# Kernel optimization log

Hardware: AMD Instinct MI355X
Metric: run time of the kernel (lower is better)

The kernel has to match this reference:

```python
import jax, jax.numpy as jnp
import numpy as np

VOCAB = 32000
HID = 1024
HEADS = 16
HEAD_DIM = HID // HEADS
LAYERS = 8
INTER = 4 * HID
ROPE_BASE = 100000.0
EPS = 1e-5


def setup_inputs() -> dict:
    key = jax.random.key(0)
    ks = jax.random.split(key, 12)
    s = 0.02
    inp = {
        'input_ids': jax.random.randint(ks[0], (2, 2048), 0, VOCAB),
        'embed_W': jax.random.normal(ks[1], (VOCAB, HID), jnp.float32) * s,
        'Wq': jax.random.normal(ks[2], (LAYERS, HID, HID), jnp.float32) * s,
        'Wk': jax.random.normal(ks[3], (LAYERS, HID, HID), jnp.float32) * s,
        'Wv': jax.random.normal(ks[4], (LAYERS, HID, HID), jnp.float32) * s,
        'Wo': jax.random.normal(ks[5], (LAYERS, HID, HID), jnp.float32) * s,
        'Wg': jax.random.normal(ks[6], (LAYERS, HID, INTER), jnp.float32) * s,
        'Wu': jax.random.normal(ks[7], (LAYERS, HID, INTER), jnp.float32) * s,
        'Wd': jax.random.normal(ks[8], (LAYERS, INTER, HID), jnp.float32) * s,
        'norm1_w': jnp.ones((LAYERS, HID), jnp.float32),
        'norm2_w': jnp.ones((LAYERS, HID), jnp.float32),
        'final_norm_w': jnp.ones((HID,), jnp.float32),
        'head_W': jax.random.normal(ks[9], (HID, VOCAB), jnp.float32) * s,
    }
    return inp


def rms_norm(x, w):
    return x * jax.lax.rsqrt(jnp.mean(x * x, axis=-1, keepdims=True) + EPS) * w


def rope_tables(seq_len):
    freq = 1.0 / (ROPE_BASE ** (jnp.arange(0, HEAD_DIM, 2, dtype=jnp.float32) / HEAD_DIM))
    ang = jnp.arange(seq_len, dtype=jnp.float32)[:, None] * freq  # [S, d/2]
    cos = jnp.concatenate([jnp.cos(ang), jnp.cos(ang)], axis=-1)  # [S, d]
    sin = jnp.concatenate([jnp.sin(ang), jnp.sin(ang)], axis=-1)
    return cos, sin


def rotate_half(x):
    h = x.shape[-1] // 2
    return jnp.concatenate([-x[..., h:], x[..., :h]], axis=-1)


def apply_rope(q, k, cos, sin):
    # q,k: [B,S,H,D]; cos,sin: [S,D] -> broadcast over heads via [:,None,:]
    c = cos[:, None, :]
    s = sin[:, None, :]
    return q * c + rotate_half(q) * s, k * c + rotate_half(k) * s


def attention(x, wq, wk, wv, wo, cos, sin, causal_mask):
    B, S, _ = x.shape
    q = (x @ wq).reshape(B, S, HEADS, HEAD_DIM)
    k = (x @ wk).reshape(B, S, HEADS, HEAD_DIM)
    v = (x @ wv).reshape(B, S, HEADS, HEAD_DIM)
    q, k = apply_rope(q, k, cos, sin)
    scores = jnp.einsum('bqhd,bkhd->bhqk', q, k) / np.sqrt(HEAD_DIM)
    scores = jnp.clip(scores, -1000.0, 1000.0)
    scores = jnp.where(causal_mask, jnp.finfo(scores.dtype).min, scores)
    w = jax.nn.softmax(scores.astype(jnp.float32), axis=-1).astype(q.dtype)
    w = jnp.clip(w, 0.0, 1.0)
    ctx = jnp.einsum('bhqk,bkhd->bqhd', w, v).reshape(B, S, HID)
    return ctx @ wo


def reference(input_ids, embed_W, Wq, Wk, Wv, Wo, Wg, Wu, Wd, norm1_w, norm2_w, final_norm_w, head_W):
    B, S = input_ids.shape
    h = embed_W[input_ids]  # [B,S,HID]
    cos, sin = rope_tables(S)
    causal_mask = jnp.triu(jnp.ones((S, S), bool), k=1)[None, None]
    for l in range(LAYERS):
        h = h + attention(rms_norm(h, norm1_w[l]), Wq[l], Wk[l], Wv[l], Wo[l], cos, sin, causal_mask)
        hn = rms_norm(h, norm2_w[l])
        h = h + (jax.nn.silu(hn @ Wg[l]) * (hn @ Wu[l])) @ Wd[l]
    h = rms_norm(h, final_norm_w)
    logits = h @ head_W
    return logits, h
```

## Files before the change

kernel.cpp:

```cpp
#include <hip/hip_runtime.h>

#define T_TOK 4096
#define SEQ   2048
#define HID   1024
#define NH    16
#define HD    64
#define INTER 4096
#define NLAYER 8
#define VOCAB 32000

typedef short short8 __attribute__((ext_vector_type(8)));
typedef float f32x4  __attribute__((ext_vector_type(4)));

__device__ __forceinline__ unsigned short f2bf(float f){
  unsigned int u = __builtin_bit_cast(unsigned int, f);
  u += 0x7fffu + ((u >> 16) & 1u);
  return (unsigned short)(u >> 16);
}
__device__ __forceinline__ float bf2f(unsigned short b){
  unsigned int u = ((unsigned int)b) << 16;
  return __builtin_bit_cast(float, u);
}

#define GLOAD_LDS16(gsrc, ldst) \
  __builtin_amdgcn_global_load_lds((const __attribute__((address_space(1))) void*)(gsrc), \
                                   (__attribute__((address_space(3))) void*)(ldst), 16, 0, 0)

__global__ __launch_bounds__(256) void embed_kernel(const int* __restrict__ ids,
                                                    const float* __restrict__ W,
                                                    float* __restrict__ h){
  int i = blockIdx.x * 256 + threadIdx.x;
  int t = i >> 8, c = i & 255;
  ((float4*)h)[i] = ((const float4*)(W + (size_t)ids[t] * HID))[c];
}

__global__ __launch_bounds__(256) void rope_tab_kernel(float* __restrict__ cosT,
                                                       float* __restrict__ sinT){
  int i = blockIdx.x * 256 + threadIdx.x;
  int s = i >> 5, f = i & 31;
  float inv = expf(-((2.0f * (float)f) / 64.0f) * logf(100000.0f));
  float ang = (float)s * inv;
  cosT[i] = cosf(ang);
  sinT[i] = sinf(ang);
}

__global__ __launch_bounds__(256) void rmsnorm_kernel(const float* __restrict__ h,
                                                      const float* __restrict__ w,
                                                      unsigned short* __restrict__ out,
                                                      float* hcopy){
  int t = blockIdx.x, tid = threadIdx.x;
  float4 v = ((const float4*)(h + (size_t)t * HID))[tid];
  float ss = v.x*v.x + v.y*v.y + v.z*v.z + v.w*v.w;
  #pragma unroll
  for (int m = 1; m < 64; m <<= 1) ss += __shfl_xor(ss, m);
  __shared__ float red[4];
  if ((tid & 63) == 0) red[tid >> 6] = ss;
  __syncthreads();
  float r = rsqrtf((red[0] + red[1] + red[2] + red[3]) * (1.0f / HID) + 1e-5f);
  float4 wv = ((const float4*)w)[tid];
  float nx = v.x * r * wv.x;
  float ny = v.y * r * wv.y;
  float nz = v.z * r * wv.z;
  float nw = v.w * r * wv.w;
  ushort4 o;
  o.x = f2bf(nx); o.y = f2bf(ny); o.z = f2bf(nz); o.w = f2bf(nw);
  ((ushort4*)(out + (size_t)t * HID))[tid] = o;
  if (hcopy){
    float4 hv; hv.x = nx; hv.y = ny; hv.z = nz; hv.w = nw;
    ((float4*)(hcopy + (size_t)t * HID))[tid] = hv;
  }
}

__global__ __launch_bounds__(256) void convert_w_qkvo(const float* __restrict__ W0,
                                                      const float* __restrict__ W1,
                                                      const float* __restrict__ W2,
                                                      const float* __restrict__ W3,
                                                      unsigned short* __restrict__ Wt){
  __shared__ unsigned short t_lds[64][72];
  const int z = blockIdx.z, sel = z >> 3, l = z & 7;
  const float* W = ((sel == 0) ? W0 : (sel == 1) ? W1 : (sel == 2) ? W2 : W3)
                 + (size_t)l * HID * HID;
  unsigned short* dst = Wt + (size_t)z * HID * HID;
  const int n0 = blockIdx.x * 64, k0 = blockIdx.y * 64;
  const int tid = threadIdx.x;
  const int tr = tid >> 4, tc = tid & 15;
  #pragma unroll
  for (int i = 0; i < 4; ++i){
    int kk = tr + i * 16;
    float4 v = *(const float4*)(W + (size_t)(k0 + kk) * HID + n0 + tc * 4);
    t_lds[tc*4+0][kk] = f2bf(v.x);
    t_lds[tc*4+1][kk] = f2bf(v.y);
    t_lds[tc*4+2][kk] = f2bf(v.z);
    t_lds[tc*4+3][kk] = f2bf(v.w);
  }
  __syncthreads();
  const int n = tid >> 2, cp = tid & 3;
  #pragma unroll
  for (int j = 0; j < 2; ++j){
    int c = cp * 2 + j;
    uint4 d = *(const uint4*)(&t_lds[n][c * 8]);
    *(uint4*)(dst + (size_t)(n0 + n) * HID + k0 + ((c ^ (n & 7)) << 3)) = d;
  }
}

__global__ __launch_bounds__(256) void convert_w_swz(const float* __restrict__ W,
                                                     unsigned short* __restrict__ Wt,
                                                     int K, int N){
  __shared__ unsigned short t_lds[64][72];
  W  += (size_t)blockIdx.z * K * N;
  Wt += (size_t)blockIdx.z * K * N;
  const int n0 = blockIdx.x * 64, k0 = blockIdx.y * 64;
  const int tid = threadIdx.x;
  const int tr = tid >> 4, tc = tid & 15;
  #pragma unroll
  for (int i = 0; i < 4; ++i){
    int kk = tr + i * 16;
    float4 v = *(const float4*)(W + (size_t)(k0 + kk) * N + n0 + tc * 4);
    t_lds[tc*4+0][kk] = f2bf(v.x);
    t_lds[tc*4+1][kk] = f2bf(v.y);
    t_lds[tc*4+2][kk] = f2bf(v.z);
    t_lds[tc*4+3][kk] = f2bf(v.w);
  }
  __syncthreads();
  const int n = tid >> 2, cp = tid & 3;
  #pragma unroll
  for (int j = 0; j < 2; ++j){
    int c = cp * 2 + j;
    uint4 d = *(const uint4*)(&t_lds[n][c * 8]);
    *(uint4*)(Wt + (size_t)(n0 + n) * K + k0 + ((c ^ (n & 7)) << 3)) = d;
  }
}

__global__ __launch_bounds__(256) void convert_w_lin(const float* __restrict__ W,
                                                     unsigned short* __restrict__ Wt,
                                                     int K, int N){
  __shared__ unsigned short t_lds[64][72];
  const int n0 = blockIdx.x * 64, k0 = blockIdx.y * 64;
  const int tid = threadIdx.x;
  const int tr = tid >> 4, tc = tid & 15;
  #pragma unroll
  for (int i = 0; i < 4; ++i){
    int kk = tr + i * 16;
    float4 v = *(const float4*)(W + (size_t)(k0 + kk) * N + n0 + tc * 4);
    t_lds[tc*4+0][kk] = f2bf(v.x);
    t_lds[tc*4+1][kk] = f2bf(v.y);
    t_lds[tc*4+2][kk] = f2bf(v.z);
    t_lds[tc*4+3][kk] = f2bf(v.w);
  }
  __syncthreads();
  const int n = tid >> 2, cp = tid & 3;
  #pragma unroll
  for (int j = 0; j < 2; ++j){
    int c = cp * 2 + j;
    uint4 d = *(const uint4*)(&t_lds[n][c * 8]);
    *(uint4*)(Wt + (size_t)(n0 + n) * K + k0 + c * 8) = d;
  }
}

__device__ __forceinline__ void gemm_core64(const unsigned short* __restrict__ A,
                                            const unsigned short* __restrict__ Bt,
                                            int K, int m0, int n0,
                                            unsigned short* As, unsigned short* Bs,
                                            f32x4 (&acc)[4][4]){
  const int tid = threadIdx.x;
  const int lane = tid & 63, w = tid >> 6;
  const int l15 = lane & 15, g = lane >> 4;
  const int lr = lane >> 3;
  const int lc = lane & 7;
  const int wr = w >> 1, wc = w & 1;
  const int axor = ((lc ^ lr) << 3);

  #pragma unroll
  for (int m = 0; m < 4; ++m)
    #pragma unroll
    for (int n = 0; n < 4; ++n)
      #pragma unroll
      for (int i = 0; i < 4; ++i) acc[m][n][i] = 0.0f;

  for (int kk = 0; kk < K; kk += 64){
    __syncthreads();
    #pragma unroll
    for (int i = 0; i < 4; ++i){
      int rb = (i * 4 + w) * 8;
      GLOAD_LDS16(A  + (size_t)(m0 + rb + lr) * K + kk + axor,      As + rb * 64);
      GLOAD_LDS16(Bt + (size_t)(n0 + rb + lr) * K + kk + (lc << 3), Bs + rb * 64);
    }
    __syncthreads();
    short8 a[4][2], b[4][2];
    const int x = l15 & 7;
    #pragma unroll
    for (int m = 0; m < 4; ++m){
      int row = wr * 64 + m * 16 + l15;
      a[m][0] = *(const short8*)(As + row * 64 + ((g       ^ x) << 3));
      a[m][1] = *(const short8*)(As + row * 64 + (((4 + g) ^ x) << 3));
    }
    #pragma unroll
    for (int n = 0; n < 4; ++n){
      int row = wc * 64 + n * 16 + l15;
      b[n][0] = *(const short8*)(Bs + row * 64 + ((g       ^ x) << 3));
      b[n][1] = *(const short8*)(Bs + row * 64 + (((4 + g) ^ x) << 3));
    }
    #pragma unroll
    for (int m = 0; m < 4; ++m)
      #pragma unroll
      for (int n = 0; n < 4; ++n){
        acc[m][n] = __builtin_amdgcn_mfma_f32_16x16x32_bf16(a[m][0], b[n][0], acc[m][n], 0, 0, 0);
        acc[m][n] = __builtin_amdgcn_mfma_f32_16x16x32_bf16(a[m][1], b[n][1], acc[m][n], 0, 0, 0);
      }
  }
}

template<int MODE>
__device__ __forceinline__ void gemm_epi(const f32x4 (&acc)[4][4], void* Cout,
                                         const float* __restrict__ resid,
                                         int N, int m0, int n0, int ldt){
  const int tid = threadIdx.x;
  const int lane = tid & 63, w = tid >> 6;
  const int l15 = lane & 15, g = lane >> 4;
  const int wr = w >> 1, wc = w & 1;
  #pragma unroll
  for (int m = 0; m < 4; ++m){
    #pragma unroll
    for (int n = 0; n < 4; ++n){
      int row0 = m0 + wr * 64 + m * 16 + g * 4;
      int col  = n0 + wc * 64 + n * 16 + l15;
      #pragma unroll
      for (int i = 0; i < 4; ++i){
        float v = acc[m][n][i];
        if (MODE == 0){
          ((unsigned short*)Cout)[(size_t)(row0 + i) * N + col] = f2bf(v);
        } else if (MODE == 1){
          size_t idx = (size_t)(row0 + i) * N + col;
          ((float*)Cout)[idx] = resid[idx] + v;
        } else if (MODE == 2){
          ((unsigned short*)Cout)[(size_t)col * ldt + (row0 + i)] = f2bf(v);
        } else {
          __builtin_nontemporal_store(v, &((float*)Cout)[(size_t)(row0 + i) * N + col]);
        }
      }
    }
  }
}

__global__ __launch_bounds__(256) void gemm_od(const unsigned short* __restrict__ A,
                                               const unsigned short* __restrict__ Bt,
                                               float* __restrict__ Cout,
                                               const float* __restrict__ resid,
                                               int K, int N){
  __shared__ unsigned short As[64 * 64];
  __shared__ unsigned short Bs[128 * 64];
  const int tid = threadIdx.x;
  const int lane = tid & 63, w = tid >> 6;
  const int l15 = lane & 15, g = lane >> 4;
  const int lr = lane >> 3, lc = lane & 7;
  const int axor = ((lc ^ lr) << 3);
  const int m0 = blockIdx.x * 64, n0 = blockIdx.y * 128;

  f32x4 acc[4][2];
  #pragma unroll
  for (int m = 0; m < 4; ++m)
    #pragma unroll
    for (int n = 0; n < 2; ++n)
      #pragma unroll
      for (int i = 0; i < 4; ++i) acc[m][n][i] = 0.0f;

  for (int kk = 0; kk < K; kk += 64){
    __syncthreads();
    #pragma unroll
    for (int i = 0; i < 2; ++i){
      int rb = (i * 4 + w) * 8;
      GLOAD_LDS16(A + (size_t)(m0 + rb + lr) * K + kk + axor, As + rb * 64);
    }
    #pragma unroll
    for (int i = 0; i < 4; ++i){
      int rb = (i * 4 + w) * 8;
      GLOAD_LDS16(Bt + (size_t)(n0 + rb + lr) * K + kk + (lc << 3), Bs + rb * 64);
    }
    __syncthreads();
    short8 a[4][2], b[2][2];
    const int x = l15 & 7;
    #pragma unroll
    for (int m = 0; m < 4; ++m){
      int row = m * 16 + l15;
      a[m][0] = *(const short8*)(As + row * 64 + ((g       ^ x) << 3));
      a[m][1] = *(const short8*)(As + row * 64 + (((4 + g) ^ x) << 3));
    }
    #pragma unroll
    for (int n = 0; n < 2; ++n){
      int row = w * 32 + n * 16 + l15;
      b[n][0] = *(const short8*)(Bs + row * 64 + ((g       ^ x) << 3));
      b[n][1] = *(const short8*)(Bs + row * 64 + (((4 + g) ^ x) << 3));
    }
    #pragma unroll
    for (int m = 0; m < 4; ++m)
      #pragma unroll
      for (int n = 0; n < 2; ++n){
        acc[m][n] = __builtin_amdgcn_mfma_f32_16x16x32_bf16(a[m][0], b[n][0], acc[m][n], 0, 0, 0);
        acc[m][n] = __builtin_amdgcn_mfma_f32_16x16x32_bf16(a[m][1], b[n][1], acc[m][n], 0, 0, 0);
      }
  }
  #pragma unroll
  for (int m = 0; m < 4; ++m)
    #pragma unroll
    for (int n = 0; n < 2; ++n){
      int row0 = m0 + m * 16 + g * 4;
      int col  = n0 + w * 32 + n * 16 + l15;
      #pragma unroll
      for (int i = 0; i < 4; ++i){
        size_t idx = (size_t)(row0 + i) * N + col;
        Cout[idx] = resid[idx] + acc[m][n][i];
      }
    }
}

#define WAITV4 asm volatile("s_waitcnt vmcnt(4)" ::: "memory")
#define WAITV2 asm volatile("s_waitcnt vmcnt(2)" ::: "memory")
#define WAITV0 asm volatile("s_waitcnt vmcnt(0)" ::: "memory")
#define HBAR() { __builtin_amdgcn_s_barrier(); asm volatile("" ::: "memory"); }

__global__ __launch_bounds__(512, 2) void gemm_head8p(const unsigned short* __restrict__ A,
                                                      const unsigned short* __restrict__ Bt,
                                                      float* __restrict__ out){
  __shared__ unsigned short smem8[65536];
  const int tid = threadIdx.x;
  const int lane = tid & 63, w = tid >> 6;
  const int l15 = lane & 15, g = lane >> 4;
  const int wr = w >> 2, wc = w & 3;
  const int lr8 = lane >> 3, lc = lane & 7;
  const int axor = ((lc ^ lr8) << 3);
  const int x = l15 & 7;
  const int sl0 = ((g ^ x) << 3), sl1 = (((4 + g) ^ x) << 3);
  const int m0 = blockIdx.x * 256, n0 = blockIdx.y * 256;
  const int K = HID, nt = HID / 64;

  f32x4 acc[8][4];
  #pragma unroll
  for (int m = 0; m < 8; ++m)
    #pragma unroll
    for (int n = 0; n < 4; ++n)
      #pragma unroll
      for (int i = 0; i < 4; ++i) acc[m][n][i] = 0.0f;

  #define STAGE_HALF(BUF, MAT, HALF, KK)                                           \
  {                                                                                \
    unsigned short* dbase = smem8 + ((((BUF)*2+(MAT))*2+(HALF)) << 13) + (w*8)*64; \
    const unsigned short* G = (MAT) ? Bt : A;                                      \
    const int brc = (MAT) ? n0 : m0;                                               \
    int r0 = w*8 + lr8, r1 = r0 + 64;                                              \
    int g0, g1;                                                                    \
    if (MAT){ g0 = brc + ((r0>>5)<<6) + ((HALF)<<5) + (r0&31);                     \
              g1 = brc + ((r1>>5)<<6) + ((HALF)<<5) + (r1&31); }                   \
    else    { g0 = brc + ((r0>>6)<<7) + ((HALF)<<6) + (r0&63);                     \
              g1 = brc + ((r1>>6)<<7) + ((HALF)<<6) + (r1&63); }                   \
    GLOAD_LDS16(G + (size_t)g0*K + (KK) + axor, dbase);                            \
    GLOAD_LDS16(G + (size_t)g1*K + (KK) + axor, dbase + 64*64);                    \
  }

  STAGE_HALF(0, 0, 0, 0)
  STAGE_HALF(0, 1, 0, 0)
  STAGE_HALF(0, 1, 1, 0)
  STAGE_HALF(0, 0, 1, 0)
  WAITV4;
  HBAR();

  for (int t = 0; t < nt; ++t){
    const int buf = t & 1, sb = buf ^ 1;
    const int kkn = (t + 1) * 64;
    const bool st = (t + 1 < nt);
    const int aB0 = ((buf*2+0)*2+0) << 13;
    const int aB1 = aB0 + 8192;
    const int bB0 = ((buf*2+1)*2+0) << 13;
    const int bB1 = bB0 + 8192;
    short8 a[4][2], b0[2][2], b1[2][2];

    #pragma unroll
    for (int m4 = 0; m4 < 4; ++m4){
      const unsigned short* p = smem8 + aB0 + (wr*64 + m4*16 + l15) * 64;
      a[m4][0] = *(const short8*)(p + sl0);
      a[m4][1] = *(const short8*)(p + sl1);
    }
    #pragma unroll
    for (int n2 = 0; n2 < 2; ++n2){
      const unsigned short* p = smem8 + bB0 + (wc*32 + n2*16 + l15) * 64;
      b0[n2][0] = *(const short8*)(p + sl0);
      b0[n2][1] = *(const short8*)(p + sl1);
    }
    if (st){ STAGE_HALF(sb, 0, 0, kkn) }
    HBAR();
    __builtin_amdgcn_s_setprio(1);
    #pragma unroll
    for (int m4 = 0; m4 < 4; ++m4)
      #pragma unroll
      for (int n2 = 0; n2 < 2; ++n2){
        acc[m4][n2] = __builtin_amdgcn_mfma_f32_16x16x32_bf16(a[m4][0], b0[n2][0], acc[m4][n2], 0, 0, 0);
        acc[m4][n2] = __builtin_amdgcn_mfma_f32_16x16x32_bf16(a[m4][1], b0[n2][1], acc[m4][n2], 0, 0, 0);
      }
    __builtin_amdgcn_s_setprio(0);
    if (st){ WAITV4; } else { WAITV2; }
    HBAR();

    #pragma unroll
    for (int n2 = 0; n2 < 2; ++n2){
      const unsigned short* p = smem8 + bB1 + (wc*32 + n2*16 + l15) * 64;
      b1[n2][0] = *(const short8*)(p + sl0);
      b1[n2][1] = *(const short8*)(p + sl1);
    }
    if (st){ STAGE_HALF(sb, 1, 0, kkn) }
    HBAR();
    __builtin_amdgcn_s_setprio(1);
    #pragma unroll
    for (int m4 = 0; m4 < 4; ++m4)
      #pragma unroll
      for (int n2 = 0; n2 < 2; ++n2){
        acc[m4][2+n2] = __builtin_amdgcn_mfma_f32_16x16x32_bf16(a[m4][0], b1[n2][0], acc[m4][2+n2], 0, 0, 0);
        acc[m4][2+n2] = __builtin_amdgcn_mfma_f32_16x16x32_bf16(a[m4][1], b1[n2][1], acc[m4][2+n2], 0, 0, 0);
      }
    __builtin_amdgcn_s_setprio(0);
    if (st){ WAITV4; } else { WAITV0; }
    HBAR();

    #pragma unroll
    for (int m4 = 0; m4 < 4; ++m4){
      const unsigned short* p = smem8 + aB1 + (wr*64 + m4*16 + l15) * 64;
      a[m4][0] = *(const short8*)(p + sl0);
      a[m4][1] = *(const short8*)(p + sl1);
    }
    if (st){ STAGE_HALF(sb, 1, 1, kkn) }
    HBAR();
    __builtin_amdgcn_s_setprio(1);
    #pragma unroll
    for (int m4 = 0; m4 < 4; ++m4)
      #pragma unroll
      for (int n2 = 0; n2 < 2; ++n2){
        acc[4+m4][n2] = __builtin_amdgcn_mfma_f32_16x16x32_bf16(a[m4][0], b0[n2][0], acc[4+m4][n2], 0, 0, 0);
        acc[4+m4][n2] = __builtin_amdgcn_mfma_f32_16x16x32_bf16(a[m4][1], b0[n2][1], acc[4+m4][n2], 0, 0, 0);
      }
    __builtin_amdgcn_s_setprio(0);
    HBAR();

    if (st){ STAGE_HALF(sb, 0, 1, kkn) }
    HBAR();
    __builtin_amdgcn_s_setprio(1);
    #pragma unroll
    for (int m4 = 0; m4 < 4; ++m4)
      #pragma unroll
      for (int n2 = 0; n2 < 2; ++n2){
        acc[4+m4][2+n2] = __builtin_amdgcn_mfma_f32_16x16x32_bf16(a[m4][0], b1[n2][0], acc[4+m4][2+n2], 0, 0, 0);
        acc[4+m4][2+n2] = __builtin_amdgcn_mfma_f32_16x16x32_bf16(a[m4][1], b1[n2][1], acc[4+m4][2+n2], 0, 0, 0);
      }
    __builtin_amdgcn_s_setprio(0);
    if (st){ WAITV4; }
    HBAR();
  }
  #undef STAGE_HALF

  #pragma unroll
  for (int m = 0; m < 8; ++m)
    #pragma unroll
    for (int n = 0; n < 4; ++n){
      int row0 = m0 + wr*128 + m*16 + g*4;
      int col  = n0 + wc*64  + n*16 + l15;
      #pragma unroll
      for (int i = 0; i < 4; ++i)
        __builtin_nontemporal_store(acc[m][n][i], &out[(size_t)(row0 + i) * VOCAB + col]);
    }
}

__global__ __launch_bounds__(256) void gemm_qkv(const unsigned short* __restrict__ A,
                                                const unsigned short* __restrict__ BtQ,
                                                const unsigned short* __restrict__ BtK,
                                                const unsigned short* __restrict__ BtV,
                                                unsigned short* qb, unsigned short* kb,
                                                unsigned short* vt,
                                                const float* __restrict__ cosT,
                                                const float* __restrict__ sinT){
  __shared__ unsigned short As[128 * 64];
  __shared__ unsigned short Bs[128 * 64];
  const int nb = blockIdx.y, sel = nb >> 3, n0 = (nb & 7) * 128;
  const unsigned short* Bt = (sel == 0) ? BtQ : (sel == 1) ? BtK : BtV;
  f32x4 acc[4][4];
  gemm_core64(A, Bt, HID, blockIdx.x * 128, n0, As, Bs, acc);
  if (sel == 2){
    gemm_epi<2>(acc, vt, nullptr, HID, blockIdx.x * 128, n0, T_TOK);
    return;
  }
  unsigned short* outp = sel ? kb : qb;
  const float qs = sel ? 1.0f : 0.125f;
  const int tid = threadIdx.x;
  const int lane = tid & 63, w = tid >> 6;
  const int l15 = lane & 15, g = lane >> 4;
  const int wr = w >> 1, wc = w & 1;
  const int m0 = blockIdx.x * 128;
  #pragma unroll
  for (int m = 0; m < 4; ++m){
    #pragma unroll
    for (int n = 0; n < 2; ++n){
      int row0 = m0 + wr * 64 + m * 16 + g * 4;
      int col  = n0 + wc * 64 + n * 16 + l15;
      int f    = (col & 63);
      #pragma unroll
      for (int i = 0; i < 4; ++i){
        int t = row0 + i, s = t & (SEQ - 1);
        float c  = cosT[s * 32 + f];
        float sn = sinT[s * 32 + f];
        float x0 = acc[m][n][i], x1 = acc[m][n + 2][i];
        outp[(size_t)t * HID + col]      = f2bf((x0 * c - x1 * sn) * qs);
        outp[(size_t)t * HID + col + 32] = f2bf((x1 * c + x0 * sn) * qs);
      }
    }
  }
}

__global__ __launch_bounds__(256) void gemm_gusilu(const unsigned short* __restrict__ A,
                                                   const unsigned short* __restrict__ BtG,
                                                   const unsigned short* __restrict__ BtU,
                                                   unsigned short* __restrict__ gb){
  __shared__ unsigned short As[128 * 64];
  __shared__ unsigned short Bs[128 * 64];
  const int m0 = blockIdx.x * 128, n0 = blockIdx.y * 128;
  f32x4 acc[4][4];
  gemm_core64(A, BtG, HID, m0, n0, As, Bs, acc);
  unsigned int gp[4][4][2];
  #pragma unroll
  for (int m = 0; m < 4; ++m)
    #pragma unroll
    for (int n = 0; n < 4; ++n){
      gp[m][n][0] = (unsigned int)f2bf(acc[m][n][0]) | ((unsigned int)f2bf(acc[m][n][1]) << 16);
      gp[m][n][1] = (unsigned int)f2bf(acc[m][n][2]) | ((unsigned int)f2bf(acc[m][n][3]) << 16);
    }
  gemm_core64(A, BtU, HID, m0, n0, As, Bs, acc);
  const int tid = threadIdx.x;
  const int lane = tid & 63, w = tid >> 6;
  const int l15 = lane & 15, g = lane >> 4;
  const int wr = w >> 1, wc = w & 1;
  #pragma unroll
  for (int m = 0; m < 4; ++m){
    #pragma unroll
    for (int n = 0; n < 4; ++n){
      int row0 = m0 + wr * 64 + m * 16 + g * 4;
      int col  = n0 + wc * 64 + n * 16 + l15;
      #pragma unroll
      for (int i = 0; i < 4; ++i){
        float gv = bf2f((unsigned short)(gp[m][n][i >> 1] >> ((i & 1) * 16)));
        float u  = acc[m][n][i];
        float s  = (gv / (1.0f + __expf(-gv))) * u;
        gb[(size_t)(row0 + i) * INTER + col] = f2bf(s);
      }
    }
  }
}

__global__ __launch_bounds__(256, 2) void gemm_f32b(const unsigned short* __restrict__ A,
                                                    const float* __restrict__ Bw,
                                                    float* __restrict__ Cout,
                                                    int M, int N, int K){
  __shared__ unsigned short As[128 * 32];
  __shared__ unsigned short Bs[128 * 32];
  const int tid = threadIdx.x;
  const int lane = tid & 63, wid = tid >> 6;
  const int l15 = lane & 15, g = lane >> 4;
  const int wr = wid >> 1, wc = wid & 1;
  const int m0 = blockIdx.x * 128, n0 = blockIdx.y * 128;
  const int bcol = tid & 127, bhalf = tid >> 7;
  f32x4 acc[4][4];
  #pragma unroll
  for (int m = 0; m < 4; ++m)
    #pragma unroll
    for (int n = 0; n < 4; ++n)
      #pragma unroll
      for (int i = 0; i < 4; ++i) acc[m][n][i] = 0.0f;
  for (int kk = 0; kk < K; kk += 32){
    __syncthreads();
    #pragma unroll
    for (int cc = 0; cc < 2; ++cc){
      int c = tid + cc * 256;
      int row = c >> 2, kc = (c & 3) << 3;
      uint4 d = *(const uint4*)(A + (size_t)(m0 + row) * K + kk + kc);
      *(uint4*)(&As[row * 32 + kc]) = d;
    }
    {
      const float* bp = Bw + (size_t)(kk + bhalf * 16) * N + n0 + bcol;
      float f[16];
      #pragma unroll
      for (int j = 0; j < 16; ++j) f[j] = bp[(size_t)j * N];
      unsigned int pk[8];
      #pragma unroll
      for (int j = 0; j < 8; ++j)
        pk[j] = (unsigned int)f2bf(f[2*j]) | ((unsigned int)f2bf(f[2*j+1]) << 16);
      int sw = (bcol >> 1) & 3;
      int c0 = ((bhalf << 1)     ) ^ sw;
      int c1 = ((bhalf << 1) | 1 ) ^ sw;
      uint4 w0; w0.x = pk[0]; w0.y = pk[1]; w0.z = pk[2]; w0.w = pk[3];
      uint4 w1; w1.x = pk[4]; w1.y = pk[5]; w1.z = pk[6]; w1.w = pk[7];
      *(uint4*)(&Bs[bcol * 32 + c0 * 8]) = w0;
      *(uint4*)(&Bs[bcol * 32 + c1 * 8]) = w1;
    }
    __syncthreads();
    short8 a[4], b[4];
    #pragma unroll
    for (int m = 0; m < 4; ++m)
      a[m] = *(const short8*)(&As[(wr*64 + m*16 + l15) * 32 + g*8]);
    #pragma unroll
    for (int n = 0; n < 4; ++n){
      int col = wc*64 + n*16 + l15;
      b[n] = *(const short8*)(&Bs[col * 32 + (g ^ ((col >> 1) & 3)) * 8]);
    }
    #pragma unroll
    for (int m = 0; m < 4; ++m)
      #pragma unroll
      for (int n = 0; n < 4; ++n)
        acc[m][n] = __builtin_amdgcn_mfma_f32_16x16x32_bf16(a[m], b[n], acc[m][n], 0, 0, 0);
  }
  #pragma unroll
  for (int m = 0; m < 4; ++m)
    #pragma unroll
    for (int n = 0; n < 4; ++n){
      int row0 = m0 + wr*64 + m*16 + g*4;
      int col  = n0 + wc*64 + n*16 + l15;
      #pragma unroll
      for (int i = 0; i < 4; ++i)
        Cout[(size_t)(row0 + i) * N + col] = acc[m][n][i];
    }
}

__global__ __launch_bounds__(512) void attn_kernel(const unsigned short* __restrict__ q,
                                                   const unsigned short* __restrict__ k,
                                                   const unsigned short* __restrict__ vt,
                                                   unsigned short* __restrict__ ctx){
  const int tid = threadIdx.x;
  const int lane = tid & 63, w = tid >> 6;
  const int l15 = lane & 15, g = lane >> 4;
  const int bx = (int)gridDim.x - 1 - (int)blockIdx.x;
  const int q0 = bx * 128 + w * 16;
  const int hh = blockIdx.y;
  const int tb = blockIdx.z * SEQ;

  __shared__ unsigned short Ks[64][72];
  __shared__ unsigned short Vs[64][72];
  __shared__ unsigned short Ps[8][16][72];

  short8 qa[2];
  #pragma unroll
  for (int kd = 0; kd < 2; ++kd)
    qa[kd] = *(const short8*)(q + (size_t)(tb + q0 + l15) * HID + hh*HD + kd*32 + g*8);

  float m_run[4], l_run[4];
  f32x4 o_acc[4];
  #pragma unroll
  for (int i = 0; i < 4; ++i){ m_run[i] = -1e30f; l_run[i] = 0.0f; }
  #pragma unroll
  for (int dt = 0; dt < 4; ++dt)
    #pragma unroll
    for (int i = 0; i < 4; ++i) o_acc[dt][i] = 0.0f;

  const int ntile = 2 * bx + 2;
  const int srow = tid >> 3, sc = (tid & 7) * 8;
  const unsigned short* kbase = k  + (size_t)(tb + srow) * HID + hh*HD + sc;
  const unsigned short* vbase = vt + (size_t)(hh*HD + srow) * T_TOK + tb + sc;

  for (int kt = 0; kt < ntile; ++kt){
    const int kv0 = kt * 64;
    __syncthreads();
    *(uint4*)(&Ks[srow][sc]) = *(const uint4*)(kbase + (size_t)kv0 * HID);
    *(uint4*)(&Vs[srow][sc]) = *(const uint4*)(vbase + kv0);
    __syncthreads();
    const int dq = q0 + 15 - kv0;
    const int nct = (dq < 0) ? 0 : min(4, (dq >> 4) + 1);
    if (nct <= 0) continue;

    float pv[4][4];
    #pragma unroll
    for (int ct = 0; ct < 4; ++ct){
      if (ct < nct){
        f32x4 scv;
        #pragma unroll
        for (int i = 0; i < 4; ++i) scv[i] = 0.0f;
        scv = __builtin_amdgcn_mfma_f32_16x16x32_bf16(qa[0],
                *(const short8*)(&Ks[ct*16 + l15][g*8]), scv, 0, 0, 0);
        scv = __builtin_amdgcn_mfma_f32_16x16x32_bf16(qa[1],
                *(const short8*)(&Ks[ct*16 + l15][32 + g*8]), scv, 0, 0, 0);
        #pragma unroll
        for (int i = 0; i < 4; ++i){
          float s = fminf(fmaxf(scv[i], -1000.0f), 1000.0f);
          int row = q0 + g*4 + i;
          int col = kv0 + ct*16 + l15;
          pv[ct][i] = (col > row) ? -1e30f : s;
        }
      } else {
        #pragma unroll
        for (int i = 0; i < 4; ++i) pv[ct][i] = -1e30f;
      }
    }
    #pragma unroll
    for (int i = 0; i < 4; ++i){
      float mx = fmaxf(fmaxf(pv[0][i], pv[1][i]), fmaxf(pv[2][i], pv[3][i]));
      #pragma unroll
      for (int msk = 1; msk < 16; msk <<= 1) mx = fmaxf(mx, __shfl_xor(mx, msk));
      if (!__all(mx <= m_run[i] + 8.0f)){
        float mnew = fmaxf(m_run[i], mx);
        float scale = __expf(m_run[i] - mnew);
        m_run[i] = mnew;
        l_run[i] *= scale;
        #pragma unroll
        for (int dt = 0; dt < 4; ++dt) o_acc[dt][i] *= scale;
      }
      float psum = 0.0f;
      #pragma unroll
      for (int ct = 0; ct < 4; ++ct){
        if (ct < nct){
          float p = __expf(pv[ct][i] - m_run[i]);
          pv[ct][i] = p; psum += p;
        } else pv[ct][i] = 0.0f;
      }
      #pragma unroll
      for (int msk = 1; msk < 16; msk <<= 1) psum += __shfl_xor(psum, msk);
      l_run[i] += psum;
    }
    #pragma unroll
    for (int ct = 0; ct < 4; ++ct)
      #pragma unroll
      for (int i = 0; i < 4; ++i)
        Ps[w][g*4 + i][ct*16 + l15] = f2bf(pv[ct][i]);
    const int nks = (nct + 1) >> 1;
    #pragma unroll
    for (int ks = 0; ks < 2; ++ks){
      if (ks < nks){
        short8 ap = *(const short8*)(&Ps[w][l15][ks*32 + g*8]);
        #pragma unroll
        for (int dt = 0; dt < 4; ++dt){
          short8 vb = *(const short8*)(&Vs[dt*16 + l15][ks*32 + g*8]);
          o_acc[dt] = __builtin_amdgcn_mfma_f32_16x16x32_bf16(ap, vb, o_acc[dt], 0, 0, 0);
        }
      }
    }
  }
  #pragma unroll
  for (int i = 0; i < 4; ++i) l_run[i] = 1.0f / l_run[i];
  #pragma unroll
  for (int dt = 0; dt < 4; ++dt)
    #pragma unroll
    for (int i = 0; i < 4; ++i){
      float o = o_acc[dt][i] * l_run[i];
      ctx[(size_t)(tb + q0 + g*4 + i) * HID + hh*HD + dt*16 + l15] = f2bf(o);
    }
}

extern "C" void kernel_launch(void* const* d_in, const int* in_sizes, int n_in,
                              void* d_out, int out_size, void* d_ws, size_t ws_size,
                              hipStream_t stream){
  const int*   ids    = (const int*)d_in[0];
  const float* embedW = (const float*)d_in[1];
  const float* Wq = (const float*)d_in[2];
  const float* Wk = (const float*)d_in[3];
  const float* Wv = (const float*)d_in[4];
  const float* Wo = (const float*)d_in[5];
  const float* Wg = (const float*)d_in[6];
  const float* Wu = (const float*)d_in[7];
  const float* Wd = (const float*)d_in[8];
  const float* n1 = (const float*)d_in[9];
  const float* n2 = (const float*)d_in[10];
  const float* nf = (const float*)d_in[11];
  const float* Wh = (const float*)d_in[12];
  float* out = (float*)d_out;

  char* scb = (char*)d_out;
  unsigned short* qb  = (unsigned short*)(scb + 0);
  unsigned short* kb  = (unsigned short*)(scb + 8388608);
  unsigned short* vtb = (unsigned short*)(scb + 16777216);
  unsigned short* ctx = (unsigned short*)(scb + 25165824);
  unsigned short* gb  = (unsigned short*)(scb + 33554432);
  float* cosT = (float*)(scb + 100663296);
  float* sinT = (float*)(scb + 100925440);
  float* h_fallback   = (float*)(scb + 104857600);
  unsigned short* WtQ = (unsigned short*)(scb + 134217728);
  unsigned short* WtK = (unsigned short*)(scb + 150994944);
  unsigned short* WtV = (unsigned short*)(scb + 167772160);
  unsigned short* WtO = (unsigned short*)(scb + 184549376);
  unsigned short* WtG = (unsigned short*)(scb + 201326592);
  unsigned short* WtU = (unsigned short*)(scb + 268435456);
  unsigned short* WtD = (unsigned short*)(scb + 335544320);

  unsigned short* xn = (unsigned short*)d_ws;
  float* h = (ws_size >= 25165824u) ? (float*)((char*)d_ws + 8388608) : h_fallback;
  unsigned short* WhT = (ws_size >= 90701824u)
                      ? (unsigned short*)((char*)d_ws + 25165824) : nullptr;

  convert_w_qkvo<<<dim3(16, 16, 32), 256, 0, stream>>>(Wq, Wk, Wv, Wo, WtQ);
  convert_w_swz<<<dim3(64, 16, 8), 256, 0, stream>>>(Wg, WtG, HID, INTER);
  convert_w_swz<<<dim3(64, 16, 8), 256, 0, stream>>>(Wu, WtU, HID, INTER);
  convert_w_swz<<<dim3(16, 64, 8), 256, 0, stream>>>(Wd, WtD, INTER, HID);
  if (WhT)
    convert_w_lin<<<dim3(500, 16, 1), 256, 0, stream>>>(Wh, WhT, HID, VOCAB);

  embed_kernel<<<4096, 256, 0, stream>>>(ids, embedW, h);
  rope_tab_kernel<<<256, 256, 0, stream>>>(cosT, sinT);

  for (int l = 0; l < NLAYER; ++l){
    rmsnorm_kernel<<<4096, 256, 0, stream>>>(h, n1 + l*HID, xn, nullptr);
    gemm_qkv<<<dim3(32, 24), 256, 0, stream>>>(xn, WtQ + (size_t)l*HID*HID,
                                               WtK + (size_t)l*HID*HID,
                                               WtV + (size_t)l*HID*HID, qb, kb, vtb,
                                               cosT, sinT);
    attn_kernel<<<dim3(16, 16, 2), 512, 0, stream>>>(qb, kb, vtb, ctx);
    gemm_od<<<dim3(64, 8), 256, 0, stream>>>(ctx, WtO + (size_t)l*HID*HID,
                                             h, h, HID, HID);
    rmsnorm_kernel<<<4096, 256, 0, stream>>>(h, n2 + l*HID, xn, nullptr);
    gemm_gusilu<<<dim3(32, 32), 256, 0, stream>>>(xn, WtG + (size_t)l*HID*INTER,
                                                  WtU + (size_t)l*HID*INTER, gb);
    gemm_od<<<dim3(64, 8), 256, 0, stream>>>(gb, WtD + (size_t)l*HID*INTER,
                                             h, h, INTER, HID);
  }

  rmsnorm_kernel<<<4096, 256, 0, stream>>>(h, nf, xn, out + 131072000);
  if (WhT)
    gemm_head8p<<<dim3(16, 125), 512, 0, stream>>>(xn, WhT, out);
  else
    gemm_f32b<<<dim3(32, 250), 256, 0, stream>>>(xn, Wh, out, T_TOK, VOCAB, HID);
}
```

Measured before the change: 3.644 ms.

## Port gate/up SiLU GEMM to 256x256 eight-wave pipelined kernel

Replaces the 128x128 gate/up GEMM with a 512-thread, 256x256-tile kernel that reuses the head GEMM's double-buffered direct-to-LDS pipeline. It runs the gate GEMM and then the up GEMM as one 32-step K loop, writing the gate result to global memory as bf16 between the two halves. The epilogue reads the gate back from global to apply SiLU and multiply. Gate/up weights are now converted with a linear (non-swizzled) transposed layout to match the new staging, at the cost of an extra global round-trip for the gate values and only 256 blocks.

```diff
diff --git a/kernel.cpp b/kernel.cpp
--- a/kernel.cpp
+++ b/kernel.cpp
@@ -131,6 +131,34 @@
   }
 }
 
+__global__ __launch_bounds__(256) void convert_w_linb(const float* __restrict__ W,
+                                                      unsigned short* __restrict__ Wt,
+                                                      int K, int N){
+  __shared__ unsigned short t_lds[64][72];
+  W  += (size_t)blockIdx.z * K * N;
+  Wt += (size_t)blockIdx.z * K * N;
+  const int n0 = blockIdx.x * 64, k0 = blockIdx.y * 64;
+  const int tid = threadIdx.x;
+  const int tr = tid >> 4, tc = tid & 15;
+  #pragma unroll
+  for (int i = 0; i < 4; ++i){
+    int kk = tr + i * 16;
+    float4 v = *(const float4*)(W + (size_t)(k0 + kk) * N + n0 + tc * 4);
+    t_lds[tc*4+0][kk] = f2bf(v.x);
+    t_lds[tc*4+1][kk] = f2bf(v.y);
+    t_lds[tc*4+2][kk] = f2bf(v.z);
+    t_lds[tc*4+3][kk] = f2bf(v.w);
+  }
+  __syncthreads();
+  const int n = tid >> 2, cp = tid & 3;
+  #pragma unroll
+  for (int j = 0; j < 2; ++j){
+    int c = cp * 2 + j;
+    uint4 d = *(const uint4*)(&t_lds[n][c * 8]);
+    *(uint4*)(Wt + (size_t)(n0 + n) * K + k0 + c * 8) = d;
+  }
+}
+
 __global__ __launch_bounds__(256) void convert_w_lin(const float* __restrict__ W,
                                                      unsigned short* __restrict__ Wt,
                                                      int K, int N){
@@ -318,6 +346,21 @@
 #define WAITV0 asm volatile("s_waitcnt vmcnt(0)" ::: "memory")
 #define HBAR() { __builtin_amdgcn_s_barrier(); asm volatile("" ::: "memory"); }
 
+#define STAGE_HALF(BUF, MAT, HALF, BP, KK)                                       \
+{                                                                                \
+  unsigned short* dbase = smem8 + ((((BUF)*2+(MAT))*2+(HALF)) << 13) + (w*8)*64; \
+  const unsigned short* G = (MAT) ? (BP) : A;                                    \
+  const int brc = (MAT) ? n0 : m0;                                               \
+  int r0 = w*8 + lr8, r1 = r0 + 64;                                              \
+  int g0, g1;                                                                    \
+  if (MAT){ g0 = brc + ((r0>>5)<<6) + ((HALF)<<5) + (r0&31);                     \
+            g1 = brc + ((r1>>5)<<6) + ((HALF)<<5) + (r1&31); }                   \
+  else    { g0 = brc + ((r0>>6)<<7) + ((HALF)<<6) + (r0&63);                     \
+            g1 = brc + ((r1>>6)<<7) + ((HALF)<<6) + (r1&63); }                   \
+  GLOAD_LDS16(G + (size_t)g0*K + (KK) + axor, dbase);                            \
+  GLOAD_LDS16(G + (size_t)g1*K + (KK) + axor, dbase + 64*64);                    \
+}
+
 __global__ __launch_bounds__(512, 2) void gemm_head8p(const unsigned short* __restrict__ A,
                                                       const unsigned short* __restrict__ Bt,
                                                       float* __restrict__ out){
@@ -341,25 +384,10 @@
       #pragma unroll
       for (int i = 0; i < 4; ++i) acc[m][n][i] = 0.0f;
 
-  #define STAGE_HALF(BUF, MAT, HALF, KK)                                           \
-  {                                                                                \
-    unsigned short* dbase = smem8 + ((((BUF)*2+(MAT))*2+(HALF)) << 13) + (w*8)*64; \
-    const unsigned short* G = (MAT) ? Bt : A;                                      \
-    const int brc = (MAT) ? n0 : m0;                                               \
-    int r0 = w*8 + lr8, r1 = r0 + 64;                                              \
-    int g0, g1;                                                                    \
-    if (MAT){ g0 = brc + ((r0>>5)<<6) + ((HALF)<<5) + (r0&31);                     \
-              g1 = brc + ((r1>>5)<<6) + ((HALF)<<5) + (r1&31); }                   \
-    else    { g0 = brc + ((r0>>6)<<7) + ((HALF)<<6) + (r0&63);                     \
-              g1 = brc + ((r1>>6)<<7) + ((HALF)<<6) + (r1&63); }                   \
-    GLOAD_LDS16(G + (size_t)g0*K + (KK) + axor, dbase);                            \
-    GLOAD_LDS16(G + (size_t)g1*K + (KK) + axor, dbase + 64*64);                    \
-  }
-
-  STAGE_HALF(0, 0, 0, 0)
-  STAGE_HALF(0, 1, 0, 0)
-  STAGE_HALF(0, 1, 1, 0)
-  STAGE_HALF(0, 0, 1, 0)
+  STAGE_HALF(0, 0, 0, Bt, 0)
+  STAGE_HALF(0, 1, 0, Bt, 0)
+  STAGE_HALF(0, 1, 1, Bt, 0)
+  STAGE_HALF(0, 0, 1, Bt, 0)
   WAITV4;
   HBAR();
 
@@ -385,7 +413,7 @@
       b0[n2][0] = *(const short8*)(p + sl0);
       b0[n2][1] = *(const short8*)(p + sl1);
     }
-    if (st){ STAGE_HALF(sb, 0, 0, kkn) }
+    if (st){ STAGE_HALF(sb, 0, 0, Bt, kkn) }
     HBAR();
     __builtin_amdgcn_s_setprio(1);
     #pragma unroll
@@ -405,7 +433,7 @@
       b1[n2][0] = *(const short8*)(p + sl0);
       b1[n2][1] = *(const short8*)(p + sl1);
     }
-    if (st){ STAGE_HALF(sb, 1, 0, kkn) }
+    if (st){ STAGE_HALF(sb, 1, 0, Bt, kkn) }
     HBAR();
     __builtin_amdgcn_s_setprio(1);
     #pragma unroll
@@ -425,7 +453,7 @@
       a[m4][0] = *(const short8*)(p + sl0);
       a[m4][1] = *(const short8*)(p + sl1);
     }
-    if (st){ STAGE_HALF(sb, 1, 1, kkn) }
+    if (st){ STAGE_HALF(sb, 1, 1, Bt, kkn) }
     HBAR();
     __builtin_amdgcn_s_setprio(1);
     #pragma unroll
@@ -438,7 +466,7 @@
     __builtin_amdgcn_s_setprio(0);
     HBAR();
 
-    if (st){ STAGE_HALF(sb, 0, 1, kkn) }
+    if (st){ STAGE_HALF(sb, 0, 1, Bt, kkn) }
     HBAR();
     __builtin_amdgcn_s_setprio(1);
     #pragma unroll
@@ -452,7 +480,6 @@
     if (st){ WAITV4; }
     HBAR();
   }
-  #undef STAGE_HALF
 
   #pragma unroll
   for (int m = 0; m < 8; ++m)
@@ -463,6 +490,160 @@
       #pragma unroll
       for (int i = 0; i < 4; ++i)
         __builtin_nontemporal_store(acc[m][n][i], &out[(size_t)(row0 + i) * VOCAB + col]);
+    }
+}
+
+__global__ __launch_bounds__(512, 2) void gemm_gusilu8p(const unsigned short* __restrict__ A,
+                                                        const unsigned short* __restrict__ BtG,
+                                                        const unsigned short* __restrict__ BtU,
+                                                        unsigned short* __restrict__ gb){
+  __shared__ unsigned short smem8[65536];
+  const int tid = threadIdx.x;
+  const int lane = tid & 63, w = tid >> 6;
+  const int l15 = lane & 15, g = lane >> 4;
+  const int wr = w >> 2, wc = w & 3;
+  const int lr8 = lane >> 3, lc = lane & 7;
+  const int axor = ((lc ^ lr8) << 3);
+  const int x = l15 & 7;
+  const int sl0 = ((g ^ x) << 3), sl1 = (((4 + g) ^ x) << 3);
+  const int m0 = blockIdx.x * 256, n0 = blockIdx.y * 256;
+  const int K = HID;
+  const int nt2 = 32;
+
+  f32x4 acc[8][4];
+  #pragma unroll
+  for (int m = 0; m < 8; ++m)
+    #pragma unroll
+    for (int n = 0; n < 4; ++n)
+      #pragma unroll
+      for (int i = 0; i < 4; ++i) acc[m][n][i] = 0.0f;
+
+  STAGE_HALF(0, 0, 0, BtG, 0)
+  STAGE_HALF(0, 1, 0, BtG, 0)
+  STAGE_HALF(0, 1, 1, BtG, 0)
+  STAGE_HALF(0, 0, 1, BtG, 0)
+  WAITV4;
+  HBAR();
+
+  for (int t = 0; t < nt2; ++t){
+    if (t == 16){
+      #pragma unroll
+      for (int m = 0; m < 8; ++m)
+        #pragma unroll
+        for (int n = 0; n < 4; ++n){
+          int row0 = m0 + wr*128 + m*16 + g*4;
+          int col  = n0 + wc*64  + n*16 + l15;
+          #pragma unroll
+          for (int i = 0; i < 4; ++i){
+            gb[(size_t)(row0 + i) * INTER + col] = f2bf(acc[m][n][i]);
+            acc[m][n][i] = 0.0f;
+          }
+        }
+    }
+    const int buf = t & 1, sb = buf ^ 1;
+    const int tn = t + 1;
+    const bool st = (tn < nt2);
+    const unsigned short* Bn = (tn < 16) ? BtG : BtU;
+    const int kkn = (tn & 15) * 64;
+    const int aB0 = ((buf*2+0)*2+0) << 13;
+    const int aB1 = aB0 + 8192;
+    const int bB0 = ((buf*2+1)*2+0) << 13;
+    const int bB1 = bB0 + 8192;
+    short8 a[4][2], b0[2][2], b1[2][2];
+
+    #pragma unroll
+    for (int m4 = 0; m4 < 4; ++m4){
+      const unsigned short* p = smem8 + aB0 + (wr*64 + m4*16 + l15) * 64;
+      a[m4][0] = *(const short8*)(p + sl0);
+      a[m4][1] = *(const short8*)(p + sl1);
+    }
+    #pragma unroll
+    for (int n2 = 0; n2 < 2; ++n2){
+      const unsigned short* p = smem8 + bB0 + (wc*32 + n2*16 + l15) * 64;
+      b0[n2][0] = *(const short8*)(p + sl0);
+      b0[n2][1] = *(const short8*)(p + sl1);
+    }
+    if (st){ STAGE_HALF(sb, 0, 0, Bn, kkn) }
+    HBAR();
+    __builtin_amdgcn_s_setprio(1);
+    #pragma unroll
+    for (int m4 = 0; m4 < 4; ++m4)
+      #pragma unroll
+      for (int n2 = 0; n2 < 2; ++n2){
+        acc[m4][n2] = __builtin_amdgcn_mfma_f32_16x16x32_bf16(a[m4][0], b0[n2][0], acc[m4][n2], 0, 0, 0);
+        acc[m4][n2] = __builtin_amdgcn_mfma_f32_16x16x32_bf16(a[m4][1], b0[n2][1], acc[m4][n2], 0, 0, 0);
+      }
+    __builtin_amdgcn_s_setprio(0);
+    if (st){ WAITV4; } else { WAITV2; }
+    HBAR();
+
+    #pragma unroll
+    for (int n2 = 0; n2 < 2; ++n2){
+      const unsigned short* p = smem8 + bB1 + (wc*32 + n2*16 + l15) * 64;
+      b1[n2][0] = *(const short8*)(p + sl0);
+      b1[n2][1] = *(const short8*)(p + sl1);
+    }
+    if (st){ STAGE_HALF(sb, 1, 0, Bn, kkn) }
+    HBAR();
+    __builtin_amdgcn_s_setprio(1);
+    #pragma unroll
+    for (int m4 = 0; m4 < 4; ++m4)
+      #pragma unroll
+      for (int n2 = 0; n2 < 2; ++n2){
+        acc[m4][2+n2] = __builtin_amdgcn_mfma_f32_16x16x32_bf16(a[m4][0], b1[n2][0], acc[m4][2+n2], 0, 0, 0);
+        acc[m4][2+n2] = __builtin_amdgcn_mfma_f32_16x16x32_bf16(a[m4][1], b1[n2][1], acc[m4][2+n2], 0, 0, 0);
+      }
+    __builtin_amdgcn_s_setprio(0);
+    if (st){ WAITV4; } else { WAITV0; }
+    HBAR();
+
+    #pragma unroll
+    for (int m4 = 0; m4 < 4; ++m4){
+      const unsigned short* p = smem8 + aB1 + (wr*64 + m4*16 + l15) * 64;
+      a[m4][0] = *(const short8*)(p + sl0);
+      a[m4][1] = *(const short8*)(p + sl1);
+    }
+    if (st){ STAGE_HALF(sb, 1, 1, Bn, kkn) }
+    HBAR();
+    __builtin_amdgcn_s_setprio(1);
+    #pragma unroll
+    for (int m4 = 0; m4 < 4; ++m4)
+      #pragma unroll
+      for (int n2 = 0; n2 < 2; ++n2){
+        acc[4+m4][n2] = __builtin_amdgcn_mfma_f32_16x16x32_bf16(a[m4][0], b0[n2][0], acc[4+m4][n2], 0, 0, 0);
+        acc[4+m4][n2] = __builtin_amdgcn_mfma_f32_16x16x32_bf16(a[m4][1], b0[n2][1], acc[4+m4][n2], 0, 0, 0);
+      }
+    __builtin_amdgcn_s_setprio(0);
+    HBAR();
+
+    if (st){ STAGE_HALF(sb, 0, 1, Bn, kkn) }
+    HBAR();
+    __builtin_amdgcn_s_setprio(1);
+    #pragma unroll
+    for (int m4 = 0; m4 < 4; ++m4)
+      #pragma unroll
+      for (int n2 = 0; n2 < 2; ++n2){
+        acc[4+m4][2+n2] = __builtin_amdgcn_mfma_f32_16x16x32_bf16(a[m4][0], b1[n2][0], acc[4+m4][2+n2], 0, 0, 0);
+        acc[4+m4][2+n2] = __builtin_amdgcn_mfma_f32_16x16x32_bf16(a[m4][1], b1[n2][1], acc[4+m4][2+n2], 0, 0, 0);
+      }
+    __builtin_amdgcn_s_setprio(0);
+    if (st){ WAITV4; }
+    HBAR();
+  }
+
+  #pragma unroll
+  for (int m = 0; m < 8; ++m)
+    #pragma unroll
+    for (int n = 0; n < 4; ++n){
+      int row0 = m0 + wr*128 + m*16 + g*4;
+      int col  = n0 + wc*64  + n*16 + l15;
+      #pragma unroll
+      for (int i = 0; i < 4; ++i){
+        size_t idx = (size_t)(row0 + i) * INTER + col;
+        float gv = bf2f(gb[idx]);
+        float s  = (gv / (1.0f + __expf(-gv))) * acc[m][n][i];
+        gb[idx] = f2bf(s);
+      }
     }
 }
 
@@ -506,45 +687,6 @@
         float x0 = acc[m][n][i], x1 = acc[m][n + 2][i];
         outp[(size_t)t * HID + col]      = f2bf((x0 * c - x1 * sn) * qs);
         outp[(size_t)t * HID + col + 32] = f2bf((x1 * c + x0 * sn) * qs);
-      }
-    }
-  }
-}
-
-__global__ __launch_bounds__(256) void gemm_gusilu(const unsigned short* __restrict__ A,
-                                                   const unsigned short* __restrict__ BtG,
-                                                   const unsigned short* __restrict__ BtU,
-                                                   unsigned short* __restrict__ gb){
-  __shared__ unsigned short As[128 * 64];
-  __shared__ unsigned short Bs[128 * 64];
-  const int m0 = blockIdx.x * 128, n0 = blockIdx.y * 128;
-  f32x4 acc[4][4];
-  gemm_core64(A, BtG, HID, m0, n0, As, Bs, acc);
-  unsigned int gp[4][4][2];
-  #pragma unroll
-  for (int m = 0; m < 4; ++m)
-    #pragma unroll
-    for (int n = 0; n < 4; ++n){
-      gp[m][n][0] = (unsigned int)f2bf(acc[m][n][0]) | ((unsigned int)f2bf(acc[m][n][1]) << 16);
-      gp[m][n][1] = (unsigned int)f2bf(acc[m][n][2]) | ((unsigned int)f2bf(acc[m][n][3]) << 16);
-    }
-  gemm_core64(A, BtU, HID, m0, n0, As, Bs, acc);
-  const int tid = threadIdx.x;
-  const int lane = tid & 63, w = tid >> 6;
-  const int l15 = lane & 15, g = lane >> 4;
-  const int wr = w >> 1, wc = w & 1;
-  #pragma unroll
-  for (int m = 0; m < 4; ++m){
-    #pragma unroll
-    for (int n = 0; n < 4; ++n){
-      int row0 = m0 + wr * 64 + m * 16 + g * 4;
-      int col  = n0 + wc * 64 + n * 16 + l15;
-      #pragma unroll
-      for (int i = 0; i < 4; ++i){
-        float gv = bf2f((unsigned short)(gp[m][n][i >> 1] >> ((i & 1) * 16)));
-        float u  = acc[m][n][i];
-        float s  = (gv / (1.0f + __expf(-gv))) * u;
-        gb[(size_t)(row0 + i) * INTER + col] = f2bf(s);
       }
     }
   }
@@ -786,8 +928,8 @@
                       ? (unsigned short*)((char*)d_ws + 25165824) : nullptr;
 
   convert_w_qkvo<<<dim3(16, 16, 32), 256, 0, stream>>>(Wq, Wk, Wv, Wo, WtQ);
-  convert_w_swz<<<dim3(64, 16, 8), 256, 0, stream>>>(Wg, WtG, HID, INTER);
-  convert_w_swz<<<dim3(64, 16, 8), 256, 0, stream>>>(Wu, WtU, HID, INTER);
+  convert_w_linb<<<dim3(64, 16, 8), 256, 0, stream>>>(Wg, WtG, HID, INTER);
+  convert_w_linb<<<dim3(64, 16, 8), 256, 0, stream>>>(Wu, WtU, HID, INTER);
   convert_w_swz<<<dim3(16, 64, 8), 256, 0, stream>>>(Wd, WtD, INTER, HID);
   if (WhT)
     convert_w_lin<<<dim3(500, 16, 1), 256, 0, stream>>>(Wh, WhT, HID, VOCAB);
@@ -805,8 +947,8 @@
     gemm_od<<<dim3(64, 8), 256, 0, stream>>>(ctx, WtO + (size_t)l*HID*HID,
                                              h, h, HID, HID);
     rmsnorm_kernel<<<4096, 256, 0, stream>>>(h, n2 + l*HID, xn, nullptr);
-    gemm_gusilu<<<dim3(32, 32), 256, 0, stream>>>(xn, WtG + (size_t)l*HID*INTER,
-                                                  WtU + (size_t)l*HID*INTER, gb);
+    gemm_gusilu8p<<<dim3(16, 16), 512, 0, stream>>>(xn, WtG + (size_t)l*HID*INTER,
+                                                    WtU + (size_t)l*HID*INTER, gb);
     gemm_od<<<dim3(64, 8), 256, 0, stream>>>(gb, WtD + (size_t)l*HID*INTER,
                                              h, h, INTER, HID);
   }
```

After: 4.128 ms. 1.13x slower.

## Coalesce V-transpose stores via LDS staging and prefetch K/V tiles in attention

Applied to the files above, without the earlier changes.

In the QKV GEMM, the V-projection epilogue now packs bf16 values into a padded shared-memory tile and writes the transposed V in two passes with 16-byte coalesced stores, replacing the scattered transposed writes. In the attention kernel, the next K/V tile is loaded into registers right after the current one is committed to shared memory, so global-load latency overlaps with the MFMA work. This costs extra syncthreads and registers in exchange for better store coalescing and latency hiding.

```diff
diff --git a/kernel.cpp b/kernel.cpp
--- a/kernel.cpp
+++ b/kernel.cpp
@@ -474,23 +474,48 @@
                                                 unsigned short* vt,
                                                 const float* __restrict__ cosT,
                                                 const float* __restrict__ sinT){
-  __shared__ unsigned short As[128 * 64];
-  __shared__ unsigned short Bs[128 * 64];
+  __shared__ unsigned short smem[128 * 64 * 2];
+  unsigned short* As = smem;
+  unsigned short* Bs = smem + 128 * 64;
   const int nb = blockIdx.y, sel = nb >> 3, n0 = (nb & 7) * 128;
   const unsigned short* Bt = (sel == 0) ? BtQ : (sel == 1) ? BtK : BtV;
+  const int m0 = blockIdx.x * 128;
   f32x4 acc[4][4];
-  gemm_core64(A, Bt, HID, blockIdx.x * 128, n0, As, Bs, acc);
-  if (sel == 2){
-    gemm_epi<2>(acc, vt, nullptr, HID, blockIdx.x * 128, n0, T_TOK);
-    return;
-  }
-  unsigned short* outp = sel ? kb : qb;
-  const float qs = sel ? 1.0f : 0.125f;
+  gemm_core64(A, Bt, HID, m0, n0, As, Bs, acc);
   const int tid = threadIdx.x;
   const int lane = tid & 63, w = tid >> 6;
   const int l15 = lane & 15, g = lane >> 4;
   const int wr = w >> 1, wc = w & 1;
-  const int m0 = blockIdx.x * 128;
+  if (sel == 2){
+    unsigned short (*T)[136] = (unsigned short(*)[136])smem;
+    #pragma unroll
+    for (int p = 0; p < 2; ++p){
+      __syncthreads();
+      if (wc == p){
+        #pragma unroll
+        for (int m = 0; m < 4; ++m)
+          #pragma unroll
+          for (int n = 0; n < 4; ++n)
+            #pragma unroll
+            for (int k2 = 0; k2 < 2; ++k2){
+              unsigned int pk = (unsigned int)f2bf(acc[m][n][2*k2])
+                              | ((unsigned int)f2bf(acc[m][n][2*k2+1]) << 16);
+              *(unsigned int*)(&T[n*16 + l15][wr*64 + m*16 + g*4 + 2*k2]) = pk;
+            }
+      }
+      __syncthreads();
+      #pragma unroll
+      for (int j = 0; j < 4; ++j){
+        int idx = tid + j * 256;
+        int colL = idx >> 4, ch = idx & 15;
+        *(uint4*)(vt + (size_t)(n0 + p*64 + colL) * T_TOK + m0 + ch*8) =
+            *(const uint4*)(&T[colL][ch*8]);
+      }
+    }
+    return;
+  }
+  unsigned short* outp = sel ? kb : qb;
+  const float qs = sel ? 1.0f : 0.125f;
   #pragma unroll
   for (int m = 0; m < 4; ++m){
     #pragma unroll
@@ -658,12 +683,19 @@
   const unsigned short* kbase = k  + (size_t)(tb + srow) * HID + hh*HD + sc;
   const unsigned short* vbase = vt + (size_t)(hh*HD + srow) * T_TOK + tb + sc;
 
+  uint4 kreg = *(const uint4*)(kbase);
+  uint4 vreg = *(const uint4*)(vbase);
+
   for (int kt = 0; kt < ntile; ++kt){
     const int kv0 = kt * 64;
     __syncthreads();
-    *(uint4*)(&Ks[srow][sc]) = *(const uint4*)(kbase + (size_t)kv0 * HID);
-    *(uint4*)(&Vs[srow][sc]) = *(const uint4*)(vbase + kv0);
+    *(uint4*)(&Ks[srow][sc]) = kreg;
+    *(uint4*)(&Vs[srow][sc]) = vreg;
     __syncthreads();
+    if (kt + 1 < ntile){
+      kreg = *(const uint4*)(kbase + (size_t)(kv0 + 64) * HID);
+      vreg = *(const uint4*)(vbase + kv0 + 64);
+    }
     const int dq = q0 + 15 - kv0;
     const int nct = (dq < 0) ? 0 : min(4, (dq >> 4) + 1);
     if (nct <= 0) continue;
```

Measured after the change: 3.558 ms. 2.4% less time.
